# Kernel optimization log

Hardware: AMD Instinct MI355X
Metric: run time of the kernel (lower is better)

Reference implementation:

```python
import jax, jax.numpy as jnp
import numpy as np


def setup_inputs() -> dict:
    key = jax.random.key(0)
    k1, k2, k3 = jax.random.split(key, 3)
    B, S, IN, OUT = 4, 2048, 4096, 11008
    x = jax.random.normal(k1, (B, S, IN), dtype=jnp.float32)
    # int8 weight values, stored as int32 (representable range [-0, 127))
    weight = jax.random.randint(k2, (OUT, IN), 0, 127, dtype=jnp.int32)
    weight_scaler = jax.random.uniform(k3, (OUT,), dtype=jnp.float32)
    return {"x": x, "weight": weight, "weight_scaler": weight_scaler}


def reference(x, weight, weight_scaler):
    # XlaQuantizedLinear per-channel weight-only quantized matmul:
    # out = (x @ w.T) * w_scaler, where int8 w is dequantized by casting
    # to the activation dtype, and per-output-channel scale applied after GEMM.
    w = weight.astype(x.dtype)                     # [OUT, IN]
    out = jnp.einsum('bsi,oi->bso', x, w)          # [B, S, OUT]
    return out * weight_scaler                     # broadcast over last dim
```

## Files before the change

kernel.cpp:

```cpp
#include <hip/hip_runtime.h>
#include <stdint.h>


typedef __attribute__((ext_vector_type(4))) int i32x4;
typedef __attribute__((ext_vector_type(4))) short short4v;
typedef __attribute__((ext_vector_type(4))) float f32x4;

#define NXCD 8
#define RSZ 16384
#define RING 81920

__device__ __forceinline__ short bf16_bits(float f) {
  uint32_t u = __builtin_bit_cast(uint32_t, f);
  uint32_t r = (u + 0x7FFFu + ((u >> 16) & 1u)) >> 16;
  return (short)r;
}

__device__ __forceinline__ void gl_lds16(const void* g, void* l) {
  __builtin_amdgcn_global_load_lds(
      (const __attribute__((address_space(1))) void*)g,
      (__attribute__((address_space(3))) void*)l, 16, 0, 0);
}

__global__ __launch_bounds__(512, 2) void gemm256i8(
    const char* __restrict__ A, const char* __restrict__ B,
    const float* __restrict__ rs, const float* __restrict__ scaler,
    float* __restrict__ C, int M, int N, int K) {
  __shared__ alignas(16) char sm[RING];

  const int tid = threadIdx.x;
  const int l = tid & 63;
  const int w = tid >> 6;
  const int wr = w >> 2, wc = w & 3;
  const int ln15 = l & 15;

  const int nwg = gridDim.x;
  const int ntn = N >> 8;
  int bid = blockIdx.x;
  int q = nwg / NXCD, rr = nwg % NXCD;
  int xcd = bid % NXCD, idx = bid / NXCD;
  int swz = (xcd < rr ? xcd * (q + 1) : rr * (q + 1) + (xcd - rr) * q) + idx;
  const int m0 = (swz / ntn) << 8, n0 = (swz % ntn) << 8;

  const size_t ldkb = (size_t)K;

  const int srow8 = l >> 3;
  const int sswz = ((l & 7) ^ srow8) << 4;
  const char* Ag = A + (size_t)(m0 + w * 8 + srow8) * ldkb + sswz;
  const char* Bg = B + (size_t)(n0 + (w >> 2) * 64 + (w & 3) * 8 + srow8) * ldkb + sswz;

  const int swzc = (l & 7) << 4;
  const int klo = (l >> 4) << 4;
  const int e45 = klo ^ (swzc & 48);
  const int s6 = swzc & 64;
  const int kof0 = e45 | s6;
  const int kof1 = e45 | (64 ^ s6);

  i32x4 acc[8][4] = {};
  i32x4 a[8], b0[4], b1[4];

  const int NT = K >> 7;

#define WRAP(x) ((x) >= RING ? (x) - RING : (x))

#define LDA8R(base, dst) do {                                                 \
    const char* _b = sm + (base) + (wr * 64 + ln15) * 128;                    \
    _Pragma("unroll") for (int f = 0; f < 4; ++f) {                           \
      dst[f*2+0] = *(const i32x4*)(_b + f*2048 + kof0);                       \
      dst[f*2+1] = *(const i32x4*)(_b + f*2048 + kof1); } } while (0)

#define LDB4R(base, dst) do {                                                 \
    const char* _b = sm + (base) + (wc * 32 + ln15) * 128;                    \
    _Pragma("unroll") for (int nf = 0; nf < 2; ++nf) {                        \
      dst[nf*2+0] = *(const i32x4*)(_b + nf*2048 + kof0);                     \
      dst[nf*2+1] = *(const i32x4*)(_b + nf*2048 + kof1); } } while (0)

#define STAGE_A(base, mh, tb) do {                                            \
    gl_lds16(Ag + (size_t)((mh)*64) * ldkb + (tb),                            \
             sm + (base) + w * 1024);                                         \
    gl_lds16(Ag + (size_t)((mh)*64 + 128) * ldkb + (tb),                      \
             sm + (base) + 8192 + w * 1024); } while (0)

#define STAGE_B(base, nh, tb) do {                                            \
    gl_lds16(Bg + (size_t)((nh)*32) * ldkb + (tb),                            \
             sm + (base) + w * 1024);                                         \
    gl_lds16(Bg + (size_t)((nh)*32 + 128) * ldkb + (tb),                      \
             sm + (base) + 8192 + w * 1024); } while (0)

#define MMAQ(mh, nh, av, bv) do {                                             \
    _Pragma("unroll") for (int f = 0; f < 4; ++f)                             \
    _Pragma("unroll") for (int nf = 0; nf < 2; ++nf)                          \
    _Pragma("unroll") for (int ks = 0; ks < 2; ++ks)                          \
      acc[(mh)*4+f][(nh)*2+nf] = __builtin_amdgcn_mfma_i32_16x16x64_i8(       \
          av[f*2+ks], bv[nf*2+ks], acc[(mh)*4+f][(nh)*2+nf], 0, 0, 0);        \
  } while (0)

#define BAR() do { __builtin_amdgcn_sched_barrier(0);                         \
    asm volatile("s_barrier" ::: "memory");                                   \
    __builtin_amdgcn_sched_barrier(0); } while (0)

#define VMW(n) asm volatile("s_waitcnt vmcnt(" #n ")" ::: "memory")

  STAGE_A(0 * RSZ, 0, 0);
  STAGE_B(1 * RSZ, 0, 0);
  STAGE_B(2 * RSZ, 1, 0);
  STAGE_A(3 * RSZ, 1, 0);
  VMW(4);
  BAR();

  {
    const size_t tb1 = 128;
    LDB4R(1 * RSZ, b0);
    LDA8R(0 * RSZ, a);
    STAGE_A(4 * RSZ, 0, tb1);
    VMW(4); BAR();
    MMAQ(0, 0, a, b0);
    LDB4R(2 * RSZ, b1);
    STAGE_B(0 * RSZ, 0, tb1);
    VMW(4); BAR();
    MMAQ(0, 1, a, b1);
    LDA8R(3 * RSZ, a);
    STAGE_B(1 * RSZ, 1, tb1);
    VMW(2); BAR();
    MMAQ(1, 0, a, b0);
    LDB4R(0 * RSZ, b0);
    STAGE_A(2 * RSZ, 1, tb1);
  }

  int rb = 4 * RSZ;

  for (int t = 1; t < NT - 1; ++t) {
    const int rA0 = rb, rB0 = WRAP(rb + RSZ), rB1 = WRAP(rb + 2 * RSZ);
    const int rA1 = WRAP(rb + 3 * RSZ), rN = WRAP(rb + 4 * RSZ);
    const size_t tbn = (size_t)(t + 1) << 7;
    VMW(4); BAR();
    MMAQ(1, 1, a, b1);
    LDA8R(rA0, a);
    STAGE_A(rN, 0, tbn);
    VMW(4); BAR();
    MMAQ(0, 0, a, b0);
    LDB4R(rB1, b1);
    STAGE_B(rA0, 0, tbn);
    VMW(4); BAR();
    MMAQ(0, 1, a, b1);
    LDA8R(rA1, a);
    STAGE_B(rB0, 1, tbn);
    VMW(2); BAR();
    MMAQ(1, 0, a, b0);
    LDB4R(rA0, b0);
    STAGE_A(rB1, 1, tbn);
    rb = rN;
  }

  {
    const int rA0 = rb, rB1 = WRAP(rb + 2 * RSZ), rA1 = WRAP(rb + 3 * RSZ);
    VMW(4); BAR();
    MMAQ(1, 1, a, b1);
    LDA8R(rA0, a);
    VMW(2); BAR();
    MMAQ(0, 0, a, b0);
    LDB4R(rB1, b1);
    VMW(0); BAR();
    MMAQ(0, 1, a, b1);
    LDA8R(rA1, a);
    BAR();
    MMAQ(1, 0, a, b0);
  }
  MMAQ(1, 1, a, b1);

  float scl[4];
#pragma unroll
  for (int ng = 0; ng < 4; ++ng)
    scl[ng] = scaler[n0 + wc * 64 + (ng >> 1) * 32 + (ng & 1) * 16 + ln15];
  const int row0 = m0 + wr * 128 + ((l >> 4) << 2);
  const int col0 = n0 + wc * 64 + ln15;
#pragma unroll
  for (int mf = 0; mf < 8; ++mf) {
    const int rbase = row0 + (mf >> 2) * 64 + (mf & 3) * 16;
#pragma unroll
    for (int j = 0; j < 4; ++j) {
      const float dr = rs[rbase + j];
      float* cp = C + (size_t)(rbase + j) * N + col0;
#pragma unroll
      for (int ng = 0; ng < 4; ++ng)
        cp[(ng >> 1) * 32 + (ng & 1) * 16] =
            (float)acc[mf][ng][j] * dr * scl[ng];
    }
  }
#undef WRAP
#undef LDA8R
#undef LDB4R
#undef STAGE_A
#undef STAGE_B
#undef MMAQ
#undef BAR
#undef VMW
}

__global__ __launch_bounds__(256) void qrow4k(const float* __restrict__ x,
                                              char* __restrict__ q,
                                              float* __restrict__ rs) {
  const int r = blockIdx.x;
  const float4* xr = (const float4*)(x + (size_t)r * 4096);
  const int tid = threadIdx.x;
  float4 v[4];
  float mx = 0.f;
#pragma unroll
  for (int i = 0; i < 4; ++i) {
    v[i] = xr[tid + 256 * i];
    mx = fmaxf(mx, fmaxf(fmaxf(fabsf(v[i].x), fabsf(v[i].y)),
                         fmaxf(fabsf(v[i].z), fabsf(v[i].w))));
  }
#pragma unroll
  for (int off = 32; off; off >>= 1) mx = fmaxf(mx, __shfl_down(mx, off));
  __shared__ float smx[4];
  __shared__ float sinv;
  if ((tid & 63) == 0) smx[tid >> 6] = mx;
  __syncthreads();
  if (tid == 0) {
    float m = fmaxf(fmaxf(smx[0], smx[1]), fmaxf(smx[2], smx[3]));
    rs[r] = m / 127.0f;
    sinv = (m > 0.f) ? 127.0f / m : 0.f;
  }
  __syncthreads();
  const float inv = sinv;
  uint32_t* qr = (uint32_t*)(q + (size_t)r * 4096);
#pragma unroll
  for (int i = 0; i < 4; ++i) {
    int a0 = (int)rintf(v[i].x * inv), a1 = (int)rintf(v[i].y * inv);
    int a2 = (int)rintf(v[i].z * inv), a3 = (int)rintf(v[i].w * inv);
    qr[tid + 256 * i] =
        (uint32_t)(a0 & 0xff) | ((uint32_t)(a1 & 0xff) << 8) |
        ((uint32_t)(a2 & 0xff) << 16) | ((uint32_t)(a3 & 0xff) << 24);
  }
}

__global__ __launch_bounds__(256) void qrow(const float* __restrict__ x,
                                            char* __restrict__ q,
                                            float* __restrict__ rs, int K) {
  const int r = blockIdx.x;
  const float* xr = x + (size_t)r * K;
  const int tid = threadIdx.x;
  const int n4 = K >> 2;
  float mx = 0.f;
  for (int i = tid; i < n4; i += 256) {
    float4 v = ((const float4*)xr)[i];
    mx = fmaxf(mx, fmaxf(fmaxf(fabsf(v.x), fabsf(v.y)),
                         fmaxf(fabsf(v.z), fabsf(v.w))));
  }
#pragma unroll
  for (int off = 32; off; off >>= 1) mx = fmaxf(mx, __shfl_down(mx, off));
  __shared__ float smx[4];
  __shared__ float sinv;
  if ((tid & 63) == 0) smx[tid >> 6] = mx;
  __syncthreads();
  if (tid == 0) {
    float m = fmaxf(fmaxf(smx[0], smx[1]), fmaxf(smx[2], smx[3]));
    rs[r] = m / 127.0f;
    sinv = (m > 0.f) ? 127.0f / m : 0.f;
  }
  __syncthreads();
  const float inv = sinv;
  uint32_t* qr = (uint32_t*)(q + (size_t)r * K);
  for (int i = tid; i < n4; i += 256) {
    float4 v = ((const float4*)xr)[i];
    int a0 = (int)rintf(v.x * inv), a1 = (int)rintf(v.y * inv);
    int a2 = (int)rintf(v.z * inv), a3 = (int)rintf(v.w * inv);
    qr[i] = (uint32_t)(a0 & 0xff) | ((uint32_t)(a1 & 0xff) << 8) |
            ((uint32_t)(a2 & 0xff) << 16) | ((uint32_t)(a3 & 0xff) << 24);
  }
}

__global__ void qw_pack(const int* __restrict__ wq, char* __restrict__ q,
                        long long n16) {
  long long i = (long long)blockIdx.x * blockDim.x + threadIdx.x;
  const long long stride = (long long)gridDim.x * blockDim.x;
  for (; i < n16; i += stride) {
    const int4* p = (const int4*)(wq + i * 16);
    uint32_t o[4];
#pragma unroll
    for (int k = 0; k < 4; ++k) {
      int4 v = p[k];
      o[k] = (uint32_t)(v.x & 0xff) | ((uint32_t)(v.y & 0xff) << 8) |
             ((uint32_t)(v.z & 0xff) << 16) | ((uint32_t)(v.w & 0xff) << 24);
    }
    uint4 pk = {o[0], o[1], o[2], o[3]};
    *(uint4*)(q + i * 16) = pk;
  }
}

#define FBM 128
#define FBN 128
#define FBK 32

__global__ __launch_bounds__(256) void gemm_fb(
    const float* __restrict__ A, const int* __restrict__ B,
    const float* __restrict__ scaler, float* __restrict__ C,
    int M, int N, int K) {
  __shared__ alignas(16) short As[FBM * FBK];
  __shared__ alignas(16) short Bs[FBN * FBK];

  const int tid = threadIdx.x;
  const int lane = tid & 63;
  const int wid = tid >> 6;
  const int wr = wid >> 1, wc = wid & 1;

  const int nwg = gridDim.x;
  const int ntn = N / FBN;
  int bid = blockIdx.x;
  int q = nwg / NXCD, r = nwg % NXCD;
  int xcd = bid % NXCD, idx = bid / NXCD;
  int swz = (xcd < r ? xcd * (q + 1) : r * (q + 1) + (xcd - r) * q) + idx;
  const int mt = swz / ntn, nt = swz % ntn;
  const int m0 = mt * FBM, n0 = nt * FBN;

  f32x4 acc[4][4] = {};
  const int kiters = K / FBK;

  for (int kt = 0; kt < kiters; ++kt) {
    const int k0 = kt * FBK;
    __syncthreads();
#pragma unroll
    for (int qq = 0; qq < 4; ++qq) {
      int chunk = qq * 256 + tid;
      int row = chunk >> 3;
      int c4 = (chunk & 7) * 4;
      float4 va = *(const float4*)&A[(size_t)(m0 + row) * K + k0 + c4];
      int4 vb = *(const int4*)&B[(size_t)(n0 + row) * K + k0 + c4];
      short4v wa, wb;
      wa[0] = bf16_bits(va.x); wa[1] = bf16_bits(va.y);
      wa[2] = bf16_bits(va.z); wa[3] = bf16_bits(va.w);
      wb[0] = bf16_bits((float)vb.x); wb[1] = bf16_bits((float)vb.y);
      wb[2] = bf16_bits((float)vb.z); wb[3] = bf16_bits((float)vb.w);
      *(short4v*)&As[row * FBK + c4] = wa;
      *(short4v*)&Bs[row * FBK + c4] = wb;
    }
    __syncthreads();
    const int ar = wr * 64 + (lane & 15);
    const int br = wc * 64 + (lane & 15);
    const int ko = (lane >> 4) * 8;
    typedef __attribute__((ext_vector_type(8))) short short8v;
    short8v av[4], bv[4];
#pragma unroll
    for (int i = 0; i < 4; ++i) {
      av[i] = *(const short8v*)&As[(ar + i * 16) * FBK + ko];
      bv[i] = *(const short8v*)&Bs[(br + i * 16) * FBK + ko];
    }
#pragma unroll
    for (int mi = 0; mi < 4; ++mi)
#pragma unroll
      for (int ni = 0; ni < 4; ++ni)
        acc[mi][ni] = __builtin_amdgcn_mfma_f32_16x16x32_bf16(
            av[mi], bv[ni], acc[mi][ni], 0, 0, 0);
  }

  float sc[4];
  const int cc0 = n0 + wc * 64 + (lane & 15);
#pragma unroll
  for (int ni = 0; ni < 4; ++ni) sc[ni] = scaler[cc0 + ni * 16];
  const int cr0 = m0 + wr * 64 + ((lane >> 4) << 2);
#pragma unroll
  for (int mi = 0; mi < 4; ++mi)
#pragma unroll
    for (int j = 0; j < 4; ++j) {
      float* crow = C + (size_t)(cr0 + mi * 16 + j) * N;
#pragma unroll
      for (int ni = 0; ni < 4; ++ni)
        crow[cc0 + ni * 16] = acc[mi][ni][j] * sc[ni];
    }
}

extern "C" void kernel_launch(void* const* d_in, const int* in_sizes, int n_in,
                              void* d_out, int out_size, void* d_ws,
                              size_t ws_size, hipStream_t stream) {
  const float* x = (const float*)d_in[0];
  const int* w = (const int*)d_in[1];
  const float* sc = (const float*)d_in[2];
  float* out = (float*)d_out;

  const long long xn = in_sizes[0];
  const long long wn = in_sizes[1];
  const int N = in_sizes[2];
  const int K = (int)(wn / N);
  const int M = (int)(xn / K);

  const size_t need = (size_t)xn + (size_t)wn + (size_t)M * 4;
  const bool okt = (M % 256 == 0) && (N % 256 == 0) && (K % 128 == 0) &&
                   (K >= 384) && (K % 4 == 0);

  if (ws_size >= need && okt) {
    char* xq = (char*)d_ws;
    char* wq = xq + xn;
    float* rs = (float*)(wq + wn);
    if (K == 4096)
      qrow4k<<<M, 256, 0, stream>>>(x, xq, rs);
    else
      qrow<<<M, 256, 0, stream>>>(x, xq, rs, K);
    qw_pack<<<2048, 256, 0, stream>>>(w, wq, wn / 16);
    const int grid = (M / 256) * (N / 256);
    gemm256i8<<<grid, 512, 0, stream>>>(xq, wq, rs, sc, out, M, N, K);
  } else {
    const int grid = (M / FBM) * (N / FBN);
    gemm_fb<<<grid, 256, 0, stream>>>(x, w, sc, out, M, N, K);
  }
}
```

Baseline: 436.3 us.

## Shrink int8 GEMM tile to 128x128 with 2-wave blocks

Replaces the 256x256-tile, 8-wave int8 MFMA GEMM with a 128x128-tile, 2-wave variant. Each wave computes a 128x64 output slice, the LDS ring is halved, and the staging and B-fragment loads and wait counts are re-plumbed to match. This gives more, smaller blocks, which may help load balance and occupancy on the many CUs. In exchange it lowers data reuse per block and raises global/L2 traffic per output.

```diff
diff --git a/kernel.cpp b/kernel.cpp
--- a/kernel.cpp
+++ b/kernel.cpp
@@ -7,8 +7,8 @@
 typedef __attribute__((ext_vector_type(4))) float f32x4;
 
 #define NXCD 8
-#define RSZ 16384
-#define RING 81920
+#define RSZ 8192
+#define RING 40960
 
 __device__ __forceinline__ short bf16_bits(float f) {
   uint32_t u = __builtin_bit_cast(uint32_t, f);
@@ -22,7 +22,7 @@
       (__attribute__((address_space(3))) void*)l, 16, 0, 0);
 }
 
-__global__ __launch_bounds__(512, 2) void gemm256i8(
+__global__ __launch_bounds__(128, 2) void gemm128i8(
     const char* __restrict__ A, const char* __restrict__ B,
     const float* __restrict__ rs, const float* __restrict__ scaler,
     float* __restrict__ C, int M, int N, int K) {
@@ -31,23 +31,22 @@
   const int tid = threadIdx.x;
   const int l = tid & 63;
   const int w = tid >> 6;
-  const int wr = w >> 2, wc = w & 3;
   const int ln15 = l & 15;
 
   const int nwg = gridDim.x;
-  const int ntn = N >> 8;
+  const int ntn = N >> 7;
   int bid = blockIdx.x;
   int q = nwg / NXCD, rr = nwg % NXCD;
   int xcd = bid % NXCD, idx = bid / NXCD;
   int swz = (xcd < rr ? xcd * (q + 1) : rr * (q + 1) + (xcd - rr) * q) + idx;
-  const int m0 = (swz / ntn) << 8, n0 = (swz % ntn) << 8;
+  const int m0 = (swz / ntn) << 7, n0 = (swz % ntn) << 7;
 
   const size_t ldkb = (size_t)K;
 
   const int srow8 = l >> 3;
   const int sswz = ((l & 7) ^ srow8) << 4;
   const char* Ag = A + (size_t)(m0 + w * 8 + srow8) * ldkb + sswz;
-  const char* Bg = B + (size_t)(n0 + (w >> 2) * 64 + (w & 3) * 8 + srow8) * ldkb + sswz;
+  const char* Bg = B + (size_t)(n0 + w * 8 + srow8) * ldkb + sswz;
 
   const int swzc = (l & 7) << 4;
   const int klo = (l >> 4) << 4;
@@ -64,28 +63,32 @@
 #define WRAP(x) ((x) >= RING ? (x) - RING : (x))
 
 #define LDA8R(base, dst) do {                                                 \
-    const char* _b = sm + (base) + (wr * 64 + ln15) * 128;                    \
+    const char* _b = sm + (base) + ln15 * 128;                                \
     _Pragma("unroll") for (int f = 0; f < 4; ++f) {                           \
       dst[f*2+0] = *(const i32x4*)(_b + f*2048 + kof0);                       \
       dst[f*2+1] = *(const i32x4*)(_b + f*2048 + kof1); } } while (0)
 
-#define LDB4R(base, dst) do {                                                 \
-    const char* _b = sm + (base) + (wc * 32 + ln15) * 128;                    \
+#define LDBLO(base, dst) do {                                                 \
+    const char* _b = sm + (base) + ln15 * 128;                                \
     _Pragma("unroll") for (int nf = 0; nf < 2; ++nf) {                        \
       dst[nf*2+0] = *(const i32x4*)(_b + nf*2048 + kof0);                     \
       dst[nf*2+1] = *(const i32x4*)(_b + nf*2048 + kof1); } } while (0)
 
+#define LDBHI(base, dst) do {                                                 \
+    const char* _b = sm + (base) + 4096 + ln15 * 128;                         \
+    _Pragma("unroll") for (int nf = 0; nf < 2; ++nf) {                        \
+      dst[nf*2+0] = *(const i32x4*)(_b + nf*2048 + kof0);                     \
+      dst[nf*2+1] = *(const i32x4*)(_b + nf*2048 + kof1); } } while (0)
+
 #define STAGE_A(base, mh, tb) do {                                            \
-    gl_lds16(Ag + (size_t)((mh)*64) * ldkb + (tb),                            \
-             sm + (base) + w * 1024);                                         \
-    gl_lds16(Ag + (size_t)((mh)*64 + 128) * ldkb + (tb),                      \
-             sm + (base) + 8192 + w * 1024); } while (0)
-
-#define STAGE_B(base, nh, tb) do {                                            \
-    gl_lds16(Bg + (size_t)((nh)*32) * ldkb + (tb),                            \
-             sm + (base) + w * 1024);                                         \
-    gl_lds16(Bg + (size_t)((nh)*32 + 128) * ldkb + (tb),                      \
-             sm + (base) + 8192 + w * 1024); } while (0)
+    _Pragma("unroll") for (int j = 0; j < 4; ++j)                             \
+      gl_lds16(Ag + (size_t)((mh)*64 + j*16) * ldkb + (tb),                   \
+               sm + (base) + w * 1024 + j * 2048); } while (0)
+
+#define STAGE_B(base, hh, tb) do {                                            \
+    _Pragma("unroll") for (int j = 0; j < 4; ++j)                             \
+      gl_lds16(Bg + (size_t)((hh)*64 + j*16) * ldkb + (tb),                   \
+               sm + (base) + w * 1024 + j * 2048); } while (0)
 
 #define MMAQ(mh, nh, av, bv) do {                                             \
     _Pragma("unroll") for (int f = 0; f < 4; ++f)                             \
@@ -108,22 +111,23 @@
   VMW(4);
   BAR();
 
+  const int rBw0 = (1 + w) * RSZ;
+
   {
     const size_t tb1 = 128;
-    LDB4R(1 * RSZ, b0);
     LDA8R(0 * RSZ, a);
+    LDBLO(rBw0, b0);
     STAGE_A(4 * RSZ, 0, tb1);
-    VMW(4); BAR();
+    BAR();
     MMAQ(0, 0, a, b0);
-    LDB4R(2 * RSZ, b1);
+    LDBHI(rBw0, b1);
     STAGE_B(0 * RSZ, 0, tb1);
-    VMW(4); BAR();
+    VMW(8); BAR();
     MMAQ(0, 1, a, b1);
     LDA8R(3 * RSZ, a);
     STAGE_B(1 * RSZ, 1, tb1);
-    VMW(2); BAR();
+    BAR();
     MMAQ(1, 0, a, b0);
-    LDB4R(0 * RSZ, b0);
     STAGE_A(2 * RSZ, 1, tb1);
   }
 
@@ -132,34 +136,38 @@
   for (int t = 1; t < NT - 1; ++t) {
     const int rA0 = rb, rB0 = WRAP(rb + RSZ), rB1 = WRAP(rb + 2 * RSZ);
     const int rA1 = WRAP(rb + 3 * RSZ), rN = WRAP(rb + 4 * RSZ);
+    const int rBw = w ? rB1 : rB0;
     const size_t tbn = (size_t)(t + 1) << 7;
     VMW(4); BAR();
     MMAQ(1, 1, a, b1);
     LDA8R(rA0, a);
+    LDBLO(rBw, b0);
     STAGE_A(rN, 0, tbn);
-    VMW(4); BAR();
+    BAR();
     MMAQ(0, 0, a, b0);
-    LDB4R(rB1, b1);
+    LDBHI(rBw, b1);
     STAGE_B(rA0, 0, tbn);
-    VMW(4); BAR();
+    VMW(8); BAR();
     MMAQ(0, 1, a, b1);
     LDA8R(rA1, a);
     STAGE_B(rB0, 1, tbn);
-    VMW(2); BAR();
+    BAR();
     MMAQ(1, 0, a, b0);
-    LDB4R(rA0, b0);
     STAGE_A(rB1, 1, tbn);
     rb = rN;
   }
 
   {
-    const int rA0 = rb, rB1 = WRAP(rb + 2 * RSZ), rA1 = WRAP(rb + 3 * RSZ);
+    const int rA0 = rb, rB0 = WRAP(rb + RSZ), rB1 = WRAP(rb + 2 * RSZ);
+    const int rA1 = WRAP(rb + 3 * RSZ);
+    const int rBw = w ? rB1 : rB0;
     VMW(4); BAR();
     MMAQ(1, 1, a, b1);
     LDA8R(rA0, a);
-    VMW(2); BAR();
+    LDBLO(rBw, b0);
+    BAR();
     MMAQ(0, 0, a, b0);
-    LDB4R(rB1, b1);
+    LDBHI(rBw, b1);
     VMW(0); BAR();
     MMAQ(0, 1, a, b1);
     LDA8R(rA1, a);
@@ -171,9 +179,9 @@
   float scl[4];
 #pragma unroll
   for (int ng = 0; ng < 4; ++ng)
-    scl[ng] = scaler[n0 + wc * 64 + (ng >> 1) * 32 + (ng & 1) * 16 + ln15];
-  const int row0 = m0 + wr * 128 + ((l >> 4) << 2);
-  const int col0 = n0 + wc * 64 + ln15;
+    scl[ng] = scaler[n0 + w * 64 + (ng >> 1) * 32 + (ng & 1) * 16 + ln15];
+  const int row0 = m0 + ((l >> 4) << 2);
+  const int col0 = n0 + w * 64 + ln15;
 #pragma unroll
   for (int mf = 0; mf < 8; ++mf) {
     const int rbase = row0 + (mf >> 2) * 64 + (mf & 3) * 16;
@@ -189,7 +197,8 @@
   }
 #undef WRAP
 #undef LDA8R
-#undef LDB4R
+#undef LDBLO
+#undef LDBHI
 #undef STAGE_A
 #undef STAGE_B
 #undef MMAQ
@@ -385,7 +394,7 @@
   const int M = (int)(xn / K);
 
   const size_t need = (size_t)xn + (size_t)wn + (size_t)M * 4;
-  const bool okt = (M % 256 == 0) && (N % 256 == 0) && (K % 128 == 0) &&
+  const bool okt = (M % 128 == 0) && (N % 128 == 0) && (K % 128 == 0) &&
                    (K >= 384) && (K % 4 == 0);
 
   if (ws_size >= need && okt) {
@@ -397,8 +406,8 @@
     else
       qrow<<<M, 256, 0, stream>>>(x, xq, rs, K);
     qw_pack<<<2048, 256, 0, stream>>>(w, wq, wn / 16);
-    const int grid = (M / 256) * (N / 256);
-    gemm256i8<<<grid, 512, 0, stream>>>(xq, wq, rs, sc, out, M, N, K);
+    const int grid = (M / 128) * (N / 128);
+    gemm128i8<<<grid, 128, 0, stream>>>(xq, wq, rs, sc, out, M, N, K);
   } else {
     const int grid = (M / FBM) * (N / FBN);
     gemm_fb<<<grid, 256, 0, stream>>>(x, w, sc, out, M, N, K);
```

New measurement: 534.6 us. 22.5% more time.
